# Kernel tuning notes

Measured on AMD Instinct MI355X. Metric: run time of the kernel, lower is better.

## Reference

```python
import jax, jax.numpy as jnp
import numpy as np

LRELU_SLOPE = 0.2
B, H, W_IN, CIN, COUT, WDIM = 16, 32, 32, 512, 512, 512


def _fcl(w, weight, bias):
    # equalized-lr linear (gain=1, lr_mult=1), bias initialized to ones
    scale = 1.0 / np.sqrt(weight.shape[0]).astype(np.float32)
    return w @ (weight * scale) + bias


def _blur_up(x):
    # FIR blur with resample_kernel [1,3,3,1], gain = up_factor**2 = 4
    f = jnp.array([1.0, 3.0, 3.0, 1.0], dtype=x.dtype)
    f = f / f.sum()
    k = jnp.outer(f, f) * 4.0  # [4,4]
    c = x.shape[-1]
    k = jnp.tile(k[:, :, None, None], (1, 1, 1, c))  # depthwise HWIO
    return jax.lax.conv_general_dilated(
        x, k, (1, 1), 'SAME',
        dimension_numbers=('NHWC', 'HWIO', 'NHWC'),
        feature_group_count=c)


def _modconv(x, s, weight, demod, up):
    # weight: [kh,kw,cin,cout]; s: [B,cin] per-sample style
    kh, kw, cin, cout = weight.shape
    wscale = 1.0 / np.sqrt(kh * kw * cin).astype(np.float32)
    wmod = (weight * wscale)[None] * s[:, None, None, :, None]  # [B,kh,kw,cin,cout]
    if demod:
        d = jax.lax.rsqrt(jnp.sum(jnp.square(wmod), axis=(1, 2, 3)) + 1e-8)  # [B,cout]
        wmod = wmod * d[:, None, None, None, :]
    if up:
        conv1 = lambda xi, wi: jax.lax.conv_transpose(
            xi[None], wi, (2, 2), 'SAME',
            dimension_numbers=('NHWC', 'HWIO', 'NHWC'))[0]
    else:
        conv1 = lambda xi, wi: jax.lax.conv_general_dilated(
            xi[None], wi, (1, 1), 'SAME',
            dimension_numbers=('NHWC', 'HWIO', 'NHWC'))[0]
    y = jax.vmap(conv1)(x, wmod)
    if up:
        y = _blur_up(y)
    return y


def _style_block(x, w, noise, fw, fb, cw, sn, b, up):
    s = _fcl(w, fw, fb)
    y = _modconv(x, s, cw, True, up)
    y = y + sn * noise + b
    return jax.nn.leaky_relu(y, LRELU_SLOPE)


def _to_rgb(x, w, fw, fb, cw, b):
    s = _fcl(w, fw, fb)
    y = _modconv(x, s, cw, False, False)  # 1x1, no demod
    y = y + b
    return jax.nn.leaky_relu(y, LRELU_SLOPE)


def setup_inputs() -> dict:
    key = jax.random.key(0)
    ks = jax.random.split(key, 12)
    d = {
        'x': jax.random.normal(ks[0], (B, H, W_IN, CIN), jnp.float32),
        'w': jax.random.normal(ks[1], (B, WDIM), jnp.float32),
        'noise1': jax.random.normal(ks[2], (B, 2 * H, 2 * W_IN, 1), jnp.float32),
        'noise2': jax.random.normal(ks[3], (B, 2 * H, 2 * W_IN, 1), jnp.float32),
        # style block 1 (up=True)
        'fcl1_w': jax.random.normal(ks[4], (WDIM, CIN), jnp.float32),
        'fcl1_b': jnp.ones((CIN,), jnp.float32),
        'conv1_w': jax.random.normal(ks[5], (3, 3, CIN, COUT), jnp.float32),
        'scale_noise1': jnp.zeros((1, 1, 1, COUT), jnp.float32) + 0.1,
        'bias1': jax.random.normal(ks[6], (COUT,), jnp.float32),
        # style block 2 (up=False)
        'fcl2_w': jax.random.normal(ks[7], (WDIM, COUT), jnp.float32),
        'fcl2_b': jnp.ones((COUT,), jnp.float32),
        'conv2_w': jax.random.normal(ks[8], (3, 3, COUT, COUT), jnp.float32),
        'scale_noise2': jnp.zeros((1, 1, 1, COUT), jnp.float32) + 0.1,
        'bias2': jax.random.normal(ks[9], (COUT,), jnp.float32),
        # toRGB
        'fclr_w': jax.random.normal(ks[10], (WDIM, COUT), jnp.float32),
        'fclr_b': jnp.ones((COUT,), jnp.float32),
        'convr_w': jax.random.normal(ks[11], (1, 1, COUT, 3), jnp.float32),
        'biasr': jnp.zeros((3,), jnp.float32),
    }
    return d


def reference(x, w, noise1, noise2,
              fcl1_w, fcl1_b, conv1_w, scale_noise1, bias1,
              fcl2_w, fcl2_b, conv2_w, scale_noise2, bias2,
              fclr_w, fclr_b, convr_w, biasr):
    x = _style_block(x, w, noise1, fcl1_w, fcl1_b, conv1_w, scale_noise1, bias1, up=True)
    x = _style_block(x, w, noise2, fcl2_w, fcl2_b, conv2_w, scale_noise2, bias2, up=False)
    rgb = _to_rgb(x, w, fclr_w, fclr_b, convr_w, biasr)
    return (x, rgb)
```

## Files before the change

### kernel.cpp

```cpp
#include <hip/hip_runtime.h>
#include <hip/hip_bf16.h>

typedef __hip_bfloat16 bf16;
typedef __attribute__((ext_vector_type(8))) __bf16 bf16x8;
typedef __attribute__((ext_vector_type(4))) float f32x4;
typedef unsigned short ushort_t;

#define NB   16
#define HIN  32
#define WIN_ 32
#define C    512
#define HO   64
#define WO   64

__device__ __forceinline__ float lrelu(float v) { return v > 0.f ? v : 0.2f * v; }
__device__ __forceinline__ unsigned short f2bu(float f) {
    union { __hip_bfloat16 h; unsigned short u; } cv;
    cv.h = __float2bfloat16(f);
    return cv.u;
}
__device__ __forceinline__ void gload16(const ushort_t* g, ushort_t* l) {
    __builtin_amdgcn_global_load_lds(
        (const __attribute__((address_space(1))) void*)g,
        (__attribute__((address_space(3))) void*)l, 16, 0, 0);
}

__global__ __launch_bounds__(256) void style3_kernel(
    const float* __restrict__ w,
    const float* __restrict__ fw1, const float* __restrict__ fb1,
    const float* __restrict__ fw2, const float* __restrict__ fb2,
    const float* __restrict__ fwr, const float* __restrict__ fbr,
    float* __restrict__ s1, float* __restrict__ s2, float* __restrict__ srgb)
{
    const int b = blockIdx.x;
    const int which = blockIdx.y;
    const float* fw = which == 0 ? fw1 : (which == 1 ? fw2 : fwr);
    const float* fb = which == 0 ? fb1 : (which == 1 ? fb2 : fbr);
    float* dst      = which == 0 ? s1  : (which == 1 ? s2  : srgb);
    __shared__ float wrow[C];
    for (int i = threadIdx.x; i < C; i += 256) wrow[i] = w[b * C + i];
    __syncthreads();
    const float scale = 0.044194173824159216f;
    for (int co = threadIdx.x; co < C; co += 256) {
        float acc = 0.f;
        for (int ci = 0; ci < C; ci++)
            acc = fmaf(wrow[ci], fw[ci * C + co], acc);
        dst[b * C + co] = acc * scale + fb[co];
    }
}

__global__ __launch_bounds__(256) void wprep2_kernel(
    const float* __restrict__ cw1, const float* __restrict__ cw2,
    ushort_t* __restrict__ wb1, ushort_t* __restrict__ wb2,
    float* __restrict__ q1, float* __restrict__ q2)
{
    const float* cw = blockIdx.z == 0 ? cw1 : cw2;
    ushort_t* wb    = blockIdx.z == 0 ? wb1 : wb2;
    float* q        = blockIdx.z == 0 ? q1  : q2;
    const int nc = blockIdx.x;
    const int ct = blockIdx.y;
    const int tid = threadIdx.x;
    __shared__ float tile[32][65];
    float qacc[8];
    #pragma unroll
    for (int p = 0; p < 8; ++p) qacc[p] = 0.f;
    const int rr = tid >> 6;
    const int cc = tid & 63;
    const int n  = tid >> 2;
    const int kq = tid & 3;
    for (int t = 0; t < 9; ++t) {
        #pragma unroll
        for (int p = 0; p < 8; ++p) {
            const int r = p * 4 + rr;
            float v = cw[((size_t)(t * C + ct * 32 + r)) * C + nc * 64 + cc];
            tile[r][cc] = v;
            qacc[p] = fmaf(v, v, qacc[p]);
        }
        __syncthreads();
        unsigned int d[4];
        #pragma unroll
        for (int j2 = 0; j2 < 4; ++j2)
            d[j2] = (unsigned int)f2bu(tile[kq * 8 + 2 * j2][n])
                  | ((unsigned int)f2bu(tile[kq * 8 + 2 * j2 + 1][n]) << 16);
        int4 w4 = { (int)d[0], (int)d[1], (int)d[2], (int)d[3] };
        *(int4*)&wb[(((size_t)t * 16 + ct) * 512 + nc * 64 + n) * 32 + kq * 8] = w4;
        __syncthreads();
    }
    #pragma unroll
    for (int p = 0; p < 8; ++p)
        q[(ct * 32 + p * 4 + rr) * C + nc * 64 + cc] = qacc[p];
}

__global__ __launch_bounds__(256) void demod3_kernel(
    const float* __restrict__ s1, const float* __restrict__ s2,
    const float* __restrict__ q1, const float* __restrict__ q2,
    float* __restrict__ g1, float* __restrict__ g2, float wscale)
{
    const float* s = blockIdx.z == 0 ? s1 : s2;
    const float* q = blockIdx.z == 0 ? q1 : q2;
    float* g       = blockIdx.z == 0 ? g1 : g2;
    const int b = blockIdx.y;
    const int co = blockIdx.x * 256 + threadIdx.x;
    __shared__ float sq[C];
    for (int i = threadIdx.x; i < C; i += 256) {
        float v = s[b * C + i];
        sq[i] = v * v;
    }
    __syncthreads();
    float acc = 0.f;
    for (int ci = 0; ci < C; ++ci)
        acc = fmaf(q[ci * C + co], sq[ci], acc);
    g[b * C + co] = wscale / sqrtf(acc * wscale * wscale + 1e-8f);
}

__global__ __launch_bounds__(128) void xprep_kernel(
    const float* __restrict__ x, const float* __restrict__ s1,
    ushort_t* __restrict__ xp)
{
    const int ix = blockIdx.x;
    const int iy = blockIdx.y;
    const int b  = blockIdx.z;
    const int c  = threadIdx.x * 4;
    int2 pk{0, 0};
    if (iy > 0 && ix > 0) {
        const float4 xv = *(const float4*)&x[(((size_t)b * HIN + iy - 1) * WIN_ + ix - 1) * C + c];
        const float4 sv = *(const float4*)&s1[b * C + c];
        pk.x = (int)f2bu(xv.x * sv.x) | ((int)f2bu(xv.y * sv.y) << 16);
        pk.y = (int)f2bu(xv.z * sv.z) | ((int)f2bu(xv.w * sv.w) << 16);
    }
    *(int2*)&xp[(((size_t)b * 33 + iy) * 33 + ix) * 512 + c] = pk;
}

__global__ __launch_bounds__(256) void zero_kernel(int4* __restrict__ p, int n16)
{
    int i = blockIdx.x * 256 + threadIdx.x;
    int4 z{0, 0, 0, 0};
    if (i < n16) p[i] = z;
}

template<int MODE>
__global__ __launch_bounds__(256, 2) void conv_mfma(
    const ushort_t* __restrict__ xin, const ushort_t* __restrict__ wb,
    const float* __restrict__ g,
    const float* __restrict__ noise, const float* __restrict__ sn,
    const float* __restrict__ bias, float* __restrict__ out, int b0)
{
    const int id  = blockIdx.x + 4 * (blockIdx.y + 16 * blockIdx.z);
    const int cpx = 8 * gridDim.z;
    const int nid = (id & 7) * cpx + (id >> 3);
    const int n0 = (nid & 3) * 128;
    const int gy = (nid >> 2) & 15;
    const int bz = nid >> 6;
    const int b  = b0 + bz;

    const int tid = threadIdx.x;
    const int lane = tid & 63, wave = tid >> 6;
    const int wr = wave >> 1, wc = wave & 1;
    const int ln15 = lane & 15, lg = lane >> 4;

    __shared__ ushort_t As[3][8192];
    __shared__ ushort_t Bs[3][4096];
    __shared__ float nzs[256];

    int ntap = 9;
    int i0 = 0, cla = 0, clc = 0, oyb = 0, nkx = 1;
    if constexpr (MODE == 1) {
        const int cl = gy >> 2;
        i0 = (gy & 3) * 8;
        cla = cl >> 1; clc = cl & 1;
        const int nky = (cla == 0) ? 2 : 1;
        nkx = (clc == 0) ? 2 : 1;
        ntap = nky * nkx;
    } else {
        oyb = gy;
        nzs[tid] = noise[(b * HO + oyb * 4 + (tid >> 6)) * WO + (tid & 63)];
    }

    int abase[4], bbase[2];
    #pragma unroll
    for (int j = 0; j < 4; ++j) {
        const int s = tid + 256 * j;
        const int m = s >> 2;
        const int qs = (s & 3) ^ ((s >> 3) & 3);
        if constexpr (MODE == 2) {
            abase[j] = ((bz * 66 + oyb * 4 + (m >> 6)) * 66 + (m & 63)) * 512 + qs * 8;
        } else {
            abase[j] = ((b * 33 + i0 + (m >> 5) + 1) * 33 + (m & 31) + 1) * 512 + qs * 8;
        }
    }
    #pragma unroll
    for (int j = 0; j < 2; ++j) {
        const int s = tid + 256 * j;
        const int qs = (s & 3) ^ ((s >> 3) & 3);
        bbase[j] = n0 * 32 + (s >> 2) * 32 + qs * 8;
    }

    auto issue = [&](int sl, int ao, int bo) {
        #pragma unroll
        for (int j = 0; j < 4; ++j)
            gload16(xin + abase[j] + ao, &As[sl][wave * 512 + j * 2048]);
        #pragma unroll
        for (int j = 0; j < 2; ++j)
            gload16(wb + bo + bbase[j], &Bs[sl][wave * 512 + j * 2048]);
    };

    auto tap1 = [&](int u, int v, int& ao, int& bo) {
        const int ky = (cla == 0) ? 2 * u : 1;
        const int kx = (clc == 0) ? 2 * v : 1;
        const int dy = (cla + ky - 2) >> 1, dx = (clc + kx - 2) >> 1;
        ao = (dy * 33 + dx) * 512;
        bo = (ky * 3 + kx) * 262144;
    };

    const int fs = (lg ^ ((ln15 >> 1) & 3)) * 8;
    int ra[8], rb[4];
    #pragma unroll
    for (int i = 0; i < 8; ++i) ra[i] = (wr * 128 + i * 16 + ln15) * 32 + fs;
    #pragma unroll
    for (int i = 0; i < 4; ++i) rb[i] = (wc * 64 + i * 16 + ln15) * 32 + fs;

    f32x4 acc[8][4];
    #pragma unroll
    for (int i = 0; i < 8; ++i)
        #pragma unroll
        for (int j = 0; j < 4; ++j) {
            f32x4 z = {0.f, 0.f, 0.f, 0.f};
            acc[i][j] = z;
        }

    int s_ci = 0, s_u = 0, s_v = 0, s_ky = 0, s_kx = 0;
    int s_ao, s_bo;
    if constexpr (MODE == 1) tap1(0, 0, s_ao, s_bo);
    else { s_ao = 0; s_bo = 0; }

    auto advance = [&]() {
        ++s_ci;
        s_ao += 32; s_bo += 16384;
        if (s_ci == 16) {
            s_ci = 0;
            if constexpr (MODE == 1) {
                if (++s_v == nkx) { s_v = 0; ++s_u; }
                tap1(s_u, s_v, s_ao, s_bo);
            } else {
                if (++s_kx == 3) { s_kx = 0; ++s_ky; }
                s_ao = (s_ky * 66 + s_kx) * 512;
                s_bo = (s_ky * 3 + s_kx) * 262144;
            }
        }
    };

    const int nstep = ntap * 16;
    issue(0, s_ao, s_bo); advance();
    issue(1, s_ao, s_bo); advance();

    int sl = 0, slp = 2;
    for (int it = 0; it < nstep; ++it) {
        if (it + 1 < nstep) asm volatile("s_waitcnt vmcnt(6)" ::: "memory");
        else                asm volatile("s_waitcnt vmcnt(0)" ::: "memory");
        __builtin_amdgcn_s_barrier();
        __builtin_amdgcn_sched_barrier(0);

        const ushort_t* __restrict__ curA = As[sl];
        const ushort_t* __restrict__ curB = Bs[sl];
        bf16x8 aF[8], bF[4];
        #pragma unroll
        for (int mi = 0; mi < 8; ++mi)
            aF[mi] = *(const bf16x8*)&curA[ra[mi]];
        #pragma unroll
        for (int ni = 0; ni < 4; ++ni)
            bF[ni] = *(const bf16x8*)&curB[rb[ni]];

        if (it + 2 < nstep) {
            issue(slp, s_ao, s_bo);
            advance();
        }

        __builtin_amdgcn_s_setprio(1);
        #pragma unroll
        for (int mi = 0; mi < 8; ++mi)
            #pragma unroll
            for (int ni = 0; ni < 4; ++ni)
                acc[mi][ni] = __builtin_amdgcn_mfma_f32_16x16x32_bf16(
                    aF[mi], bF[ni], acc[mi][ni], 0, 0, 0);
        __builtin_amdgcn_s_setprio(0);

        sl  = (sl == 2)  ? 0 : sl + 1;
        slp = (slp == 2) ? 0 : slp + 1;
    }

    #pragma unroll
    for (int ni = 0; ni < 4; ++ni) {
        const int n = n0 + wc * 64 + ni * 16 + ln15;
        const float gv = g[b * C + n];
        float snv = 0.f, bv = 0.f;
        if constexpr (MODE == 2) { snv = sn[n]; bv = bias[n]; }
        #pragma unroll
        for (int mi = 0; mi < 8; ++mi) {
            #pragma unroll
            for (int j = 0; j < 4; ++j) {
                const int m = wr * 128 + mi * 16 + lg * 4 + j;
                int oy, ox;
                if constexpr (MODE == 1) { oy = 2 * (i0 + (m >> 5)) + cla; ox = 2 * (m & 31) + clc; }
                else { oy = oyb * 4 + (m >> 6); ox = m & 63; }
                const size_t idx = ((size_t)((b * HO + oy) * WO + ox) << 9) + n;
                float v = acc[mi][ni][j] * gv;
                if constexpr (MODE == 2) v = lrelu(v + snv * nzs[m] + bv);
                out[idx] = v;
            }
        }
    }
}

__global__ __launch_bounds__(128) void blur_kernel(
    const float* __restrict__ t0, const float* __restrict__ noise1,
    const float* __restrict__ sn1, const float* __restrict__ bias1,
    const float* __restrict__ s2, ushort_t* __restrict__ x1, int b0)
{
    const int ox = blockIdx.x, oy = blockIdx.y, bq = blockIdx.z;
    const int b = b0 + bq;
    const float nz = noise1[(b * HO + oy) * WO + ox];
    const int c = threadIdx.x * 4;
    float a0 = 0.f, a1 = 0.f, a2 = 0.f, a3 = 0.f;
    const float F[4] = {1.f, 3.f, 3.f, 1.f};
    #pragma unroll
    for (int i = 0; i < 4; ++i) {
        int iy = oy + i - 1;
        if ((unsigned)iy >= (unsigned)HO) continue;
        #pragma unroll
        for (int j = 0; j < 4; ++j) {
            int ix = ox + j - 1;
            if ((unsigned)ix >= (unsigned)WO) continue;
            float wgt = F[i] * F[j];
            const float4 v = *(const float4*)&t0[((size_t)((b * HO + iy) * WO + ix) << 9) + c];
            a0 = fmaf(wgt, v.x, a0); a1 = fmaf(wgt, v.y, a1);
            a2 = fmaf(wgt, v.z, a2); a3 = fmaf(wgt, v.w, a3);
        }
    }
    const float4 sv = *(const float4*)&sn1[c];
    const float4 bv = *(const float4*)&bias1[c];
    const float4 s2v = *(const float4*)&s2[b * C + c];
    a0 = lrelu(fmaf(sv.x, nz, a0 * 0.0625f) + bv.x) * s2v.x;
    a1 = lrelu(fmaf(sv.y, nz, a1 * 0.0625f) + bv.y) * s2v.y;
    a2 = lrelu(fmaf(sv.z, nz, a2 * 0.0625f) + bv.z) * s2v.z;
    a3 = lrelu(fmaf(sv.w, nz, a3 * 0.0625f) + bv.w) * s2v.w;
    int2 pk;
    pk.x = (int)f2bu(a0) | ((int)f2bu(a1) << 16);
    pk.y = (int)f2bu(a2) | ((int)f2bu(a3) << 16);
    *(int2*)&x1[(((size_t)bq * 66 + oy + 1) * 66 + ox + 1) * 512 + c] = pk;
}

__global__ __launch_bounds__(256) void torgb2_kernel(
    const float* __restrict__ x2, const float* __restrict__ srgb,
    const float* __restrict__ wr, const float* __restrict__ biasr,
    float* __restrict__ rgb)
{
    const int b = blockIdx.y;
    const int tid = threadIdx.x;
    __shared__ float weff[C][3];
    const float scale = 0.044194173824159216f;
    for (int ci = tid; ci < C; ci += 256) {
        float sc = scale * srgb[b * C + ci];
        weff[ci][0] = sc * wr[ci * 3 + 0];
        weff[ci][1] = sc * wr[ci * 3 + 1];
        weff[ci][2] = sc * wr[ci * 3 + 2];
    }
    __syncthreads();
    const int l16 = tid & 15;
    const int px  = blockIdx.x * 16 + (tid >> 4);
    const float* base = x2 + ((size_t)(b * 4096 + px) << 9);
    float a0 = 0.f, a1 = 0.f, a2 = 0.f;
    #pragma unroll
    for (int i = 0; i < 8; ++i) {
        const int c = i * 64 + l16 * 4;
        const float4 v = *(const float4*)&base[c];
        a0 = fmaf(v.x, weff[c][0], a0);     a1 = fmaf(v.x, weff[c][1], a1);     a2 = fmaf(v.x, weff[c][2], a2);
        a0 = fmaf(v.y, weff[c+1][0], a0);   a1 = fmaf(v.y, weff[c+1][1], a1);   a2 = fmaf(v.y, weff[c+1][2], a2);
        a0 = fmaf(v.z, weff[c+2][0], a0);   a1 = fmaf(v.z, weff[c+2][1], a1);   a2 = fmaf(v.z, weff[c+2][2], a2);
        a0 = fmaf(v.w, weff[c+3][0], a0);   a1 = fmaf(v.w, weff[c+3][1], a1);   a2 = fmaf(v.w, weff[c+3][2], a2);
    }
    #pragma unroll
    for (int off = 1; off < 16; off <<= 1) {
        a0 += __shfl_xor(a0, off, 16);
        a1 += __shfl_xor(a1, off, 16);
        a2 += __shfl_xor(a2, off, 16);
    }
    if (l16 < 3) {
        float v = l16 == 0 ? a0 : (l16 == 1 ? a1 : a2);
        rgb[(size_t)(b * 4096 + px) * 3 + l16] = lrelu(v + biasr[l16]);
    }
}

extern "C" void kernel_launch(void* const* d_in, const int* in_sizes, int n_in,
                              void* d_out, int out_size, void* d_ws, size_t ws_size,
                              hipStream_t stream)
{
    (void)in_sizes; (void)n_in; (void)out_size; (void)ws_size;
    const float* x       = (const float*)d_in[0];
    const float* w       = (const float*)d_in[1];
    const float* noise1  = (const float*)d_in[2];
    const float* noise2  = (const float*)d_in[3];
    const float* fcl1_w  = (const float*)d_in[4];
    const float* fcl1_b  = (const float*)d_in[5];
    const float* conv1_w = (const float*)d_in[6];
    const float* sn1     = (const float*)d_in[7];
    const float* bias1   = (const float*)d_in[8];
    const float* fcl2_w  = (const float*)d_in[9];
    const float* fcl2_b  = (const float*)d_in[10];
    const float* conv2_w = (const float*)d_in[11];
    const float* sn2     = (const float*)d_in[12];
    const float* bias2   = (const float*)d_in[13];
    const float* fclr_w  = (const float*)d_in[14];
    const float* fclr_b  = (const float*)d_in[15];
    const float* convr_w = (const float*)d_in[16];
    const float* biasr   = (const float*)d_in[17];

    float* out_x2  = (float*)d_out;
    float* out_rgb = out_x2 + 33554432;

    ushort_t* wb1 = (ushort_t*)d_ws;
    ushort_t* wb2 = wb1 + 2359296;
    ushort_t* xsp = wb1 + 4718592;
    ushort_t* x1b = xsp + 8921088;
    float* scr = (float*)(x1b + 17842176);
    float* s1   = scr;
    float* s2   = scr + 8192;
    float* g1   = scr + 16384;
    float* g2   = scr + 24576;
    float* srgb = scr + 32768;
    float* q1   = scr + 40960;
    float* q2   = scr + 303104;

    float* t0 = out_x2;

    const float WS33 = 0.014731391274719739f;

    style3_kernel<<<dim3(NB, 3), 256, 0, stream>>>(
        w, fcl1_w, fcl1_b, fcl2_w, fcl2_b, fclr_w, fclr_b, s1, s2, srgb);
    wprep2_kernel<<<dim3(8, 16, 2), 256, 0, stream>>>(conv1_w, conv2_w, wb1, wb2, q1, q2);
    demod3_kernel<<<dim3(2, NB, 2), 256, 0, stream>>>(s1, s2, q1, q2, g1, g2, WS33);
    xprep_kernel<<<dim3(33, 33, NB), 128, 0, stream>>>(x, s1, xsp);
    zero_kernel<<<8713, 256, 0, stream>>>((int4*)x1b, 2230272);

    conv_mfma<1><<<dim3(4, 16, NB), 256, 0, stream>>>(
        xsp, wb1, g1, nullptr, nullptr, nullptr, t0, 0);

    for (int half = 0; half < 2; ++half) {
        blur_kernel<<<dim3(WO, HO, 8), 128, 0, stream>>>(
            t0, noise1, sn1, bias1, s2, x1b, half * 8);
        conv_mfma<2><<<dim3(4, 16, 8), 256, 0, stream>>>(
            x1b, wb2, g2, noise2, sn2, bias2, out_x2, half * 8);
    }

    torgb2_kernel<<<dim3(256, NB), 256, 0, stream>>>(out_x2, srgb, convr_w, biasr, out_rgb);
}
```

Measured before the change: 758.7 us.

## Store upsampled conv intermediate in bf16 and tile blur through LDS

After: 678.7 us. -10.6%, faster.

```diff
diff --git a/kernel.cpp b/kernel.cpp
--- a/kernel.cpp
+++ b/kernel.cpp
@@ -113,29 +113,43 @@
     g[b * C + co] = wscale / sqrtf(acc * wscale * wscale + 1e-8f);
 }
 
-__global__ __launch_bounds__(128) void xprep_kernel(
+__global__ __launch_bounds__(256) void xprep_kernel(
     const float* __restrict__ x, const float* __restrict__ s1,
     ushort_t* __restrict__ xp)
 {
-    const int ix = blockIdx.x;
-    const int iy = blockIdx.y;
-    const int b  = blockIdx.z;
-    const int c  = threadIdx.x * 4;
+    const int u = blockIdx.x * 256 + threadIdx.x;
+    if (u >= 16 * 1089 * 128) return;
+    const int c4 = (u & 127) * 4;
+    const int p  = u >> 7;
+    const int b  = p / 1089;
+    const int r  = p - b * 1089;
+    const int iy = r / 33;
+    const int ix = r - iy * 33;
     int2 pk{0, 0};
     if (iy > 0 && ix > 0) {
-        const float4 xv = *(const float4*)&x[(((size_t)b * HIN + iy - 1) * WIN_ + ix - 1) * C + c];
-        const float4 sv = *(const float4*)&s1[b * C + c];
+        const float4 xv = *(const float4*)&x[(((size_t)b * HIN + iy - 1) * WIN_ + ix - 1) * C + c4];
+        const float4 sv = *(const float4*)&s1[b * C + c4];
         pk.x = (int)f2bu(xv.x * sv.x) | ((int)f2bu(xv.y * sv.y) << 16);
         pk.y = (int)f2bu(xv.z * sv.z) | ((int)f2bu(xv.w * sv.w) << 16);
     }
-    *(int2*)&xp[(((size_t)b * 33 + iy) * 33 + ix) * 512 + c] = pk;
-}
-
-__global__ __launch_bounds__(256) void zero_kernel(int4* __restrict__ p, int n16)
-{
-    int i = blockIdx.x * 256 + threadIdx.x;
+    *(int2*)&xp[(size_t)p * 512 + c4] = pk;
+}
+
+__global__ __launch_bounds__(256) void zero_halo_kernel(ushort_t* __restrict__ x1)
+{
+    const int u = blockIdx.x * 256 + threadIdx.x;
+    if (u >= 8 * 260 * 64) return;
+    const int bq = u / 16640;
+    const int r  = u - bq * 16640;
+    const int pi = r >> 6;
+    const int cq = (r & 63) * 8;
+    int yy, xx;
+    if (pi < 66)       { yy = 0;        xx = pi; }
+    else if (pi < 132) { yy = 65;       xx = pi - 66; }
+    else if (pi < 196) { yy = pi - 131; xx = 0;  }
+    else               { yy = pi - 195; xx = 65; }
     int4 z{0, 0, 0, 0};
-    if (i < n16) p[i] = z;
+    *(int4*)&x1[(((size_t)bq * 66 + yy) * 66 + xx) * 512 + cq] = z;
 }
 
 template<int MODE>
@@ -288,6 +302,7 @@
         slp = (slp == 2) ? 0 : slp + 1;
     }
 
+    ushort_t* outb = (ushort_t*)out;
     #pragma unroll
     for (int ni = 0; ni < 4; ++ni) {
         const int n = n0 + wc * 64 + ni * 16 + ln15;
@@ -299,54 +314,91 @@
             #pragma unroll
             for (int j = 0; j < 4; ++j) {
                 const int m = wr * 128 + mi * 16 + lg * 4 + j;
-                int oy, ox;
-                if constexpr (MODE == 1) { oy = 2 * (i0 + (m >> 5)) + cla; ox = 2 * (m & 31) + clc; }
-                else { oy = oyb * 4 + (m >> 6); ox = m & 63; }
-                const size_t idx = ((size_t)((b * HO + oy) * WO + ox) << 9) + n;
-                float v = acc[mi][ni][j] * gv;
-                if constexpr (MODE == 2) v = lrelu(v + snv * nzs[m] + bv);
-                out[idx] = v;
+                if constexpr (MODE == 1) {
+                    const int oy = 2 * (i0 + (m >> 5)) + cla;
+                    const int ox = 2 * (m & 31) + clc;
+                    const size_t idx = ((size_t)((b * HO + oy) * WO + ox) << 9) + n;
+                    outb[idx] = f2bu(acc[mi][ni][j] * gv);
+                } else {
+                    const int oy = oyb * 4 + (m >> 6);
+                    const int ox = m & 63;
+                    const size_t idx = ((size_t)((b * HO + oy) * WO + ox) << 9) + n;
+                    float v = acc[mi][ni][j] * gv;
+                    out[idx] = lrelu(v + snv * nzs[m] + bv);
+                }
             }
         }
     }
 }
 
-__global__ __launch_bounds__(128) void blur_kernel(
-    const float* __restrict__ t0, const float* __restrict__ noise1,
+__global__ __launch_bounds__(256) void blur_kernel(
+    const ushort_t* __restrict__ t0b, const float* __restrict__ noise1,
     const float* __restrict__ sn1, const float* __restrict__ bias1,
     const float* __restrict__ s2, ushort_t* __restrict__ x1, int b0)
 {
-    const int ox = blockIdx.x, oy = blockIdx.y, bq = blockIdx.z;
-    const int b = b0 + bq;
-    const float nz = noise1[(b * HO + oy) * WO + ox];
-    const int c = threadIdx.x * 4;
-    float a0 = 0.f, a1 = 0.f, a2 = 0.f, a3 = 0.f;
-    const float F[4] = {1.f, 3.f, 3.f, 1.f};
-    #pragma unroll
-    for (int i = 0; i < 4; ++i) {
-        int iy = oy + i - 1;
-        if ((unsigned)iy >= (unsigned)HO) continue;
-        #pragma unroll
-        for (int j = 0; j < 4; ++j) {
-            int ix = ox + j - 1;
-            if ((unsigned)ix >= (unsigned)WO) continue;
-            float wgt = F[i] * F[j];
-            const float4 v = *(const float4*)&t0[((size_t)((b * HO + iy) * WO + ix) << 9) + c];
-            a0 = fmaf(wgt, v.x, a0); a1 = fmaf(wgt, v.y, a1);
-            a2 = fmaf(wgt, v.z, a2); a3 = fmaf(wgt, v.w, a3);
-        }
-    }
-    const float4 sv = *(const float4*)&sn1[c];
-    const float4 bv = *(const float4*)&bias1[c];
-    const float4 s2v = *(const float4*)&s2[b * C + c];
-    a0 = lrelu(fmaf(sv.x, nz, a0 * 0.0625f) + bv.x) * s2v.x;
-    a1 = lrelu(fmaf(sv.y, nz, a1 * 0.0625f) + bv.y) * s2v.y;
-    a2 = lrelu(fmaf(sv.z, nz, a2 * 0.0625f) + bv.z) * s2v.z;
-    a3 = lrelu(fmaf(sv.w, nz, a3 * 0.0625f) + bv.w) * s2v.w;
-    int2 pk;
-    pk.x = (int)f2bu(a0) | ((int)f2bu(a1) << 16);
-    pk.y = (int)f2bu(a2) | ((int)f2bu(a3) << 16);
-    *(int2*)&x1[(((size_t)bq * 66 + oy + 1) * 66 + ox + 1) * 512 + c] = pk;
+    const int cb = blockIdx.x;
+    const int oy = blockIdx.y;
+    const int bq = blockIdx.z;
+    const int b  = b0 + bq;
+    const int tid = threadIdx.x;
+    const int c0 = cb * 128;
+
+    __shared__ ushort_t sm[4][68][128];
+    __shared__ float prm[3][128];
+
+    if (tid < 128) {
+        prm[0][tid] = sn1[c0 + tid];
+        prm[1][tid] = bias1[c0 + tid];
+        prm[2][tid] = s2[b * C + c0 + tid];
+    }
+    #pragma unroll
+    for (int rr = 0; rr < 4; ++rr) {
+        const int iy = oy + rr - 1;
+        const bool valid = (unsigned)iy < (unsigned)HO;
+        #pragma unroll
+        for (int l = 0; l < 4; ++l) {
+            const int unit = tid + l * 256;
+            const int px = unit >> 4, q = (unit & 15) * 8;
+            int4 v{0, 0, 0, 0};
+            if (valid)
+                v = *(const int4*)&t0b[(((size_t)b * HO + iy) * WO + px) * 512 + c0 + q];
+            *(int4*)&sm[rr][px + 1][q] = v;
+        }
+    }
+    {
+        const int si = tid >> 6, rr = (tid >> 4) & 3, qq = (tid & 15) * 8;
+        const int ps[4] = {0, 65, 66, 67};
+        int4 z{0, 0, 0, 0};
+        *(int4*)&sm[rr][ps[si]][qq] = z;
+    }
+    __syncthreads();
+
+    const float F2[4] = {1.f, 3.f, 3.f, 1.f};
+    #pragma unroll
+    for (int l = 0; l < 4; ++l) {
+        const int unit = tid + l * 256;
+        const int px = unit >> 4, q = (unit & 15) * 8;
+        float acc[8] = {0.f, 0.f, 0.f, 0.f, 0.f, 0.f, 0.f, 0.f};
+        #pragma unroll
+        for (int i = 0; i < 4; ++i)
+            #pragma unroll
+            for (int j = 0; j < 4; ++j) {
+                const float wgt = F2[i] * F2[j];
+                bf16x8 v = *(const bf16x8*)&sm[i][px + j][q];
+                #pragma unroll
+                for (int e = 0; e < 8; ++e)
+                    acc[e] = fmaf(wgt, (float)v[e], acc[e]);
+            }
+        const float nz = noise1[(b * HO + oy) * WO + px];
+        ushort_t ov[8];
+        #pragma unroll
+        for (int e = 0; e < 8; ++e) {
+            const int c = q + e;
+            float vv = lrelu(fmaf(prm[0][c], nz, acc[e] * 0.0625f) + prm[1][c]) * prm[2][c];
+            ov[e] = f2bu(vv);
+        }
+        *(int4*)&x1[(((size_t)bq * 66 + oy + 1) * 66 + (px + 1)) * 512 + c0 + q] = *(const int4*)ov;
+    }
 }
 
 __global__ __launch_bounds__(256) void torgb2_kernel(
@@ -417,6 +469,8 @@
     float* out_x2  = (float*)d_out;
     float* out_rgb = out_x2 + 33554432;
 
+    ushort_t* t0b = (ushort_t*)(out_x2 + 16777216);
+
     ushort_t* wb1 = (ushort_t*)d_ws;
     ushort_t* wb2 = wb1 + 2359296;
     ushort_t* xsp = wb1 + 4718592;
@@ -430,23 +484,21 @@
     float* q1   = scr + 40960;
     float* q2   = scr + 303104;
 
-    float* t0 = out_x2;
-
     const float WS33 = 0.014731391274719739f;
 
     style3_kernel<<<dim3(NB, 3), 256, 0, stream>>>(
         w, fcl1_w, fcl1_b, fcl2_w, fcl2_b, fclr_w, fclr_b, s1, s2, srgb);
     wprep2_kernel<<<dim3(8, 16, 2), 256, 0, stream>>>(conv1_w, conv2_w, wb1, wb2, q1, q2);
     demod3_kernel<<<dim3(2, NB, 2), 256, 0, stream>>>(s1, s2, q1, q2, g1, g2, WS33);
-    xprep_kernel<<<dim3(33, 33, NB), 128, 0, stream>>>(x, s1, xsp);
-    zero_kernel<<<8713, 256, 0, stream>>>((int4*)x1b, 2230272);
+    xprep_kernel<<<8712, 256, 0, stream>>>(x, s1, xsp);
+    zero_halo_kernel<<<520, 256, 0, stream>>>(x1b);
 
     conv_mfma<1><<<dim3(4, 16, NB), 256, 0, stream>>>(
-        xsp, wb1, g1, nullptr, nullptr, nullptr, t0, 0);
+        xsp, wb1, g1, nullptr, nullptr, nullptr, (float*)t0b, 0);
 
     for (int half = 0; half < 2; ++half) {
-        blur_kernel<<<dim3(WO, HO, 8), 128, 0, stream>>>(
-            t0, noise1, sn1, bias1, s2, x1b, half * 8);
+        blur_kernel<<<dim3(4, HO, 8), 256, 0, stream>>>(
+            t0b, noise1, sn1, bias1, s2, x1b, half * 8);
         conv_mfma<2><<<dim3(4, 16, 8), 256, 0, stream>>>(
             x1b, wb2, g2, noise2, sn2, bias2, out_x2, half * 8);
     }
```
